# Kernel tuning notes

Measured on AMD Instinct MI355X. Metric: run time of the kernel, lower is better.

## Reference

```python
import jax, jax.numpy as jnp
import numpy as np

NUM_HEADS = 12  # per init_kwargs


def setup_inputs() -> dict:
    key = jax.random.key(0)
    k1, k2, k3 = jax.random.split(key, 3)
    B, H, W, D = 1, 64, 64, 768
    x = jax.random.normal(k1, (B, H, W, D), dtype=jnp.float32)
    # torch nn.Linear weights are [out, in]; small init keeps softmax well-conditioned
    w_qkv = jax.random.normal(k2, (3 * D, D), dtype=jnp.float32) * 0.02
    w_proj = jax.random.normal(k3, (D, D), dtype=jnp.float32) * 0.02
    b_proj = jnp.zeros((D,), dtype=jnp.float32)
    return {"x": x, "w_qkv": w_qkv, "w_proj": w_proj, "b_proj": b_proj}


def reference(x, w_qkv, w_proj, b_proj):
    B, H, W, D = x.shape
    S = H * W
    nh = NUM_HEADS
    hd = D // nh
    scale = hd ** (-0.5)
    # qkv: [B, S, 3, nh, hd] -> q,k,v each [B, nh, S, hd]
    qkv = jnp.einsum('bhwd,ed->bhwe', x, w_qkv).reshape(B, S, 3, nh, hd)
    qkv = jnp.transpose(qkv, (2, 0, 3, 1, 4))
    q, k, v = qkv[0], qkv[1], qkv[2]
    # full O(S^2) attention matrix, as in the original module
    wei = jnp.einsum('bnqd,bnkd->bnqk', q * scale, k)
    wei = jax.nn.softmax(wei, axis=-1)
    # att_drop omitted (eval mode / deterministic baseline)
    out = jnp.einsum('bnqk,bnkd->bnqd', wei, v)  # [B, nh, S, hd]
    # [B, nh, H, W, hd] -> [B, H, W, nh*hd]
    out = jnp.transpose(out.reshape(B, nh, H, W, hd), (0, 2, 3, 1, 4)).reshape(B, H, W, D)
    proj = jnp.einsum('bhwd,ed->bhwe', out, w_proj) + b_proj
    return proj
```

## Files before the change

### kernel.cpp

```cpp
#include <hip/hip_runtime.h>
#include <hip/hip_bf16.h>
#include <math.h>

typedef short s16x8 __attribute__((ext_vector_type(8)));
typedef unsigned u32x2 __attribute__((ext_vector_type(2)));
typedef unsigned u32x4 __attribute__((ext_vector_type(4)));
typedef float f32x4 __attribute__((ext_vector_type(4)));
typedef float f32x16 __attribute__((ext_vector_type(16)));
typedef __hip_bfloat16 bf16;

#define GLD16(g, l)                                                        \
  __builtin_amdgcn_global_load_lds(                                        \
      (const __attribute__((address_space(1))) void*)(g),                  \
      (__attribute__((address_space(3))) void*)(l), 16, 0, 0)

#define MFMA16(a, b, c) __builtin_amdgcn_mfma_f32_16x16x32_bf16((a), (b), (c), 0, 0, 0)
#define MFMA32(a, b, c) __builtin_amdgcn_mfma_f32_32x32x16_bf16((a), (b), (c), 0, 0, 0)

static constexpr int kS = 4096;
static constexpr int kD = 768;
static constexpr int kNH = 12;
static constexpr int kHD = 64;
static constexpr int kNE = 2304;
static constexpr int kNS = 2;

static __device__ __forceinline__ float bf2f(short s) {
  union { unsigned u; float f; } x;
  x.u = ((unsigned)(unsigned short)s) << 16;
  return x.f;
}

static constexpr int kNX8 = kS * kD / 8;
static constexpr int kNWq8 = kNE * kD / 8;
static constexpr int kNWp8 = kD * kD / 8;

__global__ __launch_bounds__(256)
void k_cvt3(const float* __restrict__ x, const float* __restrict__ wq,
            const float* __restrict__ wp, bf16* __restrict__ xb,
            bf16* __restrict__ wqb, bf16* __restrict__ wpb) {
  int i = blockIdx.x * 256 + threadIdx.x;
  const float* src;
  short* dst;
  if (i < kNX8) {
    src = x; dst = (short*)xb;
  } else if (i < kNX8 + kNWq8) {
    i -= kNX8; src = wq; dst = (short*)wqb;
  } else {
    i -= kNX8 + kNWq8; if (i >= kNWp8) return;
    src = wp; dst = (short*)wpb;
  }
  const f32x4 a = *(const f32x4*)(src + i * 8);
  const f32x4 b = *(const f32x4*)(src + i * 8 + 4);
  s16x8 o;
#pragma unroll
  for (int j = 0; j < 4; ++j) {
    o[j] = (short)__bfloat16_as_ushort(__float2bfloat16(a[j]));
    o[j + 4] = (short)__bfloat16_as_ushort(__float2bfloat16(b[j]));
  }
  *(s16x8*)(dst + i * 8) = o;
}

__global__ __launch_bounds__(256, 2)
void k_qkv(const bf16* __restrict__ X, const bf16* __restrict__ W,
           bf16* __restrict__ Qw, bf16* __restrict__ Kw, bf16* __restrict__ Vw) {
  __shared__ __align__(16) short As[2][128 * 32];
  __shared__ __align__(16) short Bs[2][128 * 32];
  const int tid = threadIdx.x;
  const int wv = tid >> 6, ln = tid & 63;
  const int r = ln & 15, kq = ln >> 4;
  const int bm = blockIdx.x * 128;
  const int bn = blockIdx.y * 128;
  const int wr = wv >> 1, wc = wv & 1;
  const short* Xs = (const short*)X;
  const short* Ws = (const short*)W;

  f32x4 acc[4][4] = {};

  const int c0 = wv * 128 + ln, c1 = c0 + 64;
  const int ra0 = c0 >> 2, ka0 = c0 & 3;
  const int ra1 = c1 >> 2, ka1 = c1 & 3;
  const int off0 = wv * 1024, off1 = off0 + 512;
  const short* gA0 = Xs + (bm + ra0) * kD + ka0 * 8;
  const short* gA1 = Xs + (bm + ra1) * kD + ka1 * 8;
  const short* gB0 = Ws + (bn + ra0) * kD + ka0 * 8;
  const short* gB1 = Ws + (bn + ra1) * kD + ka1 * 8;

  GLD16(gA0, &As[0][off0]);
  GLD16(gA1, &As[0][off1]);
  GLD16(gB0, &Bs[0][off0]);
  GLD16(gB1, &Bs[0][off1]);
  __syncthreads();

  const int NT = kD / 32;
  for (int t = 0; t < NT; ++t) {
    const short* aCur = As[t & 1];
    const short* bCur = Bs[t & 1];
    if (t + 1 < NT) {
      const int k1 = (t + 1) * 32;
      short* aN = As[(t + 1) & 1];
      short* bN = Bs[(t + 1) & 1];
      GLD16(gA0 + k1, aN + off0);
      GLD16(gA1 + k1, aN + off1);
      GLD16(gB0 + k1, bN + off0);
      GLD16(gB1 + k1, bN + off1);
    }
    s16x8 a[4], b[4];
#pragma unroll
    for (int i = 0; i < 4; ++i)
      a[i] = *(const s16x8*)(aCur + (wr * 64 + i * 16 + r) * 32 + kq * 8);
#pragma unroll
    for (int j = 0; j < 4; ++j)
      b[j] = *(const s16x8*)(bCur + (wc * 64 + j * 16 + r) * 32 + kq * 8);
#pragma unroll
    for (int i = 0; i < 4; ++i)
#pragma unroll
      for (int j = 0; j < 4; ++j) acc[i][j] = MFMA16(a[i], b[j], acc[i][j]);
    __syncthreads();
  }

  const int which = bn / kD;
  bf16* dst = (which == 0) ? Qw : (which == 1) ? Kw : Vw;
  const float scl = (which == 0) ? 0.125f : 1.0f;
  const int ebase = bn - which * kD + wc * 64;
#pragma unroll
  for (int j = 0; j < 4; ++j) {
    const int e = ebase + j * 16 + r;
    const int h = e >> 6, d = e & 63;
#pragma unroll
    for (int i = 0; i < 4; ++i) {
      const int srow = bm + wr * 64 + i * 16 + kq * 4;
#pragma unroll
      for (int rr = 0; rr < 4; ++rr)
        dst[(h * kS + srow + rr) * kHD + d] = __float2bfloat16(acc[i][j][rr] * scl);
    }
  }
}

__global__ __launch_bounds__(256, 2)
void k_vt(const bf16* __restrict__ Vw, bf16* __restrict__ Vt) {
  __shared__ __align__(16) short L[64 * 72];
  const int h = blockIdx.y, st = blockIdx.x;
  const int t = threadIdx.x;
  const short* src = (const short*)Vw + (h * kS + st * 64) * kHD;
  short* dstb = (short*)Vt + h * kHD * kS;
#pragma unroll
  for (int u = 0; u < 2; ++u) {
    const int c = u * 256 + t;
    const int row = c >> 3, ch = c & 7;
    *(s16x8*)(L + row * 72 + ch * 8) = *(const s16x8*)(src + row * kHD + ch * 8);
  }
  __syncthreads();
#pragma unroll
  for (int u = 0; u < 2; ++u) {
    const int c = u * 256 + t;
    const int d = c >> 3, ch = c & 7;
    s16x8 v;
#pragma unroll
    for (int j = 0; j < 8; ++j) v[j] = L[(ch * 8 + j) * 72 + d];
    *(s16x8*)(dstb + d * kS + st * 64 + ch * 8) = v;
  }
}

__global__ __launch_bounds__(256, 5)
void k_attn(const bf16* __restrict__ Qw, const bf16* __restrict__ Kw,
            const bf16* __restrict__ Vt, bf16* __restrict__ Opart,
            float* __restrict__ Lpart) {
  __shared__ __align__(16) short Ks[2][64 * 64];
  __shared__ __align__(16) short Vs[2][64 * 64];
  const int tid = threadIdx.x;
  const int wv = tid >> 6, ln = tid & 63;
  const int qh = wv >> 1;
  const int kvh = wv & 1;
  const int col = ln & 31;
  const int lh = ln >> 5;

  const int wg = blockIdx.x;
  const int p = (wg & 7) >> 1;
  const int b = ((wg >> 3) << 1) | (wg & 1);
  const int hh = 3 * p + (b >> 7);
  const int rem = b & 127;
  const int qb = rem >> 1;
  const int j = rem & 1;
  const int q0 = qb * 64;
  const int pidx = (hh * 64 + qb) * kNS + j;

  const short* Qh = (const short*)Qw + ((size_t)hh * kS + q0 + qh * 32) * kHD;
  const short* Kh = (const short*)Kw + (size_t)hh * kS * kHD + (size_t)j * 2048 * kHD;
  const short* Vh = (const short*)Vt + (size_t)hh * kHD * kS + j * 2048;

  s16x8 bq[4];
#pragma unroll
  for (int kb = 0; kb < 4; ++kb)
    bq[kb] = *(const s16x8*)(Qh + col * kHD + kb * 16 + lh * 8);

  f32x16 o[2] = {};
  float lp = 0.f;

  int ldso[2];
  const short* gK[2];
  const short* gV[2];
#pragma unroll
  for (int u = 0; u < 2; ++u) {
    const int c = u * 256 + tid;
    const int kr = c >> 3, g = (c & 7) ^ (kr & 7);
    ldso[u] = c * 8;
    gK[u] = Kh + kr * kHD + g * 8;
    gV[u] = Vh + kr * kS + g * 8;
  }

#pragma unroll
  for (int u = 0; u < 2; ++u) {
    GLD16(gK[u], &Ks[0][ldso[u]]);
    GLD16(gV[u], &Vs[0][ldso[u]]);
  }
  __syncthreads();

  const int NT2 = 32;
  for (int kt = 0; kt < NT2; ++kt) {
    const short* ksCur = Ks[kt & 1];
    const short* vsCur = Vs[kt & 1];
    if (kt + 1 < NT2) {
      short* ksN = Ks[(kt + 1) & 1];
      short* vsN = Vs[(kt + 1) & 1];
      const int dk = (kt + 1) * 64 * kHD;
      const int dv = (kt + 1) * 64;
#pragma unroll
      for (int u = 0; u < 2; ++u) {
        GLD16(gK[u] + dk, ksN + ldso[u]);
        GLD16(gV[u] + dv, vsN + ldso[u]);
      }
    }

    f32x16 z = {};
    const int krow = kvh * 32 + col;
    const int ksw = krow & 7;
    __builtin_amdgcn_s_setprio(1);
#pragma unroll
    for (int kb = 0; kb < 4; ++kb) {
      const int ch = ((kb << 1) + lh) ^ ksw;
      s16x8 ak = *(const s16x8*)(ksCur + krow * 64 + ch * 8);
      z = MFMA32(ak, bq[kb], z);
    }
    __builtin_amdgcn_s_setprio(0);

    float pv[16];
#pragma unroll
    for (int g = 0; g < 16; ++g) {
      pv[g] = __expf(z[g]);
      lp += pv[g];
    }
    unsigned own[8];
#pragma unroll
    for (int m = 0; m < 8; ++m) {
      const unsigned f0 = __builtin_bit_cast(unsigned, pv[2 * m]);
      const unsigned f1 = __builtin_bit_cast(unsigned, pv[2 * m + 1]);
      own[m] = __builtin_amdgcn_perm(f1, f0, 0x07060302u);
    }

    __builtin_amdgcn_s_setprio(1);
#pragma unroll
    for (int kvk = 0; kvk < 2; ++kvk) {
      u32x2 sA = __builtin_amdgcn_permlane32_swap(own[4 * kvk + 0], own[4 * kvk + 2], false, false);
      u32x2 sB = __builtin_amdgcn_permlane32_swap(own[4 * kvk + 1], own[4 * kvk + 3], false, false);
      u32x4 apv;
      apv[0] = sA[0];
      apv[1] = sB[0];
      apv[2] = sA[1];
      apv[3] = sB[1];
      const s16x8 ap = __builtin_bit_cast(s16x8, apv);
      const int kvg = kvh * 2 + kvk;
#pragma unroll
      for (int db = 0; db < 2; ++db) {
        const int vrow = db * 32 + col;
        const int ch = ((kvg << 1) + lh) ^ (vrow & 7);
        s16x8 vb = *(const s16x8*)(vsCur + vrow * 64 + ch * 8);
        o[db] = MFMA32(ap, vb, o[db]);
      }
    }
    __builtin_amdgcn_s_setprio(0);
    __syncthreads();
  }

  lp += __shfl_xor(lp, 32);
  float* Of = (float*)Ks;
  float* Lf = (float*)Vs;

  if (kvh == 1) {
#pragma unroll
    for (int db = 0; db < 2; ++db)
#pragma unroll
      for (int g = 0; g < 16; ++g) {
        const int qoff = (g & 3) + 8 * (g >> 2) + 4 * lh;
        Of[(qh * 32 + qoff) * 64 + db * 32 + col] = o[db][g];
      }
    if (lh == 0) Lf[qh * 32 + col] = lp;
  }
  __syncthreads();
  if (kvh == 0) {
    lp += Lf[qh * 32 + col];
    if (lh == 0) Lpart[pidx * 64 + qh * 32 + col] = lp;
    short* Ob = (short*)Opart + (size_t)pidx * 4096;
#pragma unroll
    for (int db = 0; db < 2; ++db)
#pragma unroll
      for (int g = 0; g < 16; ++g) {
        const int qoff = (g & 3) + 8 * (g >> 2) + 4 * lh;
        const float val = o[db][g] + Of[(qh * 32 + qoff) * 64 + db * 32 + col];
        Ob[(qh * 32 + qoff) * 64 + db * 32 + col] =
            (short)__bfloat16_as_ushort(__float2bfloat16(val));
      }
  }
}

__global__ __launch_bounds__(256)
void k_comb(bf16* __restrict__ Opart, const float* __restrict__ Lpart) {
  const int blk = blockIdx.x;
  const int t = threadIdx.x;
  const int q = t >> 2;
  const int dg = t & 3;
  const int p0 = blk * kNS;
  const float inv = 1.0f / (Lpart[p0 * 64 + q] + Lpart[(p0 + 1) * 64 + q]);
  short* s0 = (short*)Opart + (size_t)p0 * 4096 + q * 64 + dg * 16;
  const short* s1 = s0 + 4096;
#pragma unroll
  for (int jj = 0; jj < 2; ++jj) {
    const s16x8 a = *(const s16x8*)(s0 + jj * 8);
    const s16x8 bb = *(const s16x8*)(s1 + jj * 8);
    s16x8 r;
#pragma unroll
    for (int e = 0; e < 8; ++e) {
      const float v = (bf2f(a[e]) + bf2f(bb[e])) * inv;
      r[e] = (short)__bfloat16_as_ushort(__float2bfloat16(v));
    }
    *(s16x8*)(s0 + jj * 8) = r;
  }
}

__global__ __launch_bounds__(256, 3)
void k_proj(const bf16* __restrict__ Opart, const bf16* __restrict__ W,
            const float* __restrict__ Bias, float* __restrict__ Out) {
  __shared__ __align__(16) short As[2][64 * 32];
  __shared__ __align__(16) short Bs[2][64 * 32];
  const int tid = threadIdx.x;
  const int wv = tid >> 6, ln = tid & 63;
  const int r = ln & 15, kq = ln >> 4;
  const int bm = blockIdx.x * 64;
  const int bn = blockIdx.y * 64;
  const int wr = wv >> 1, wc = wv & 1;
  const short* Asrc = (const short*)Opart;
  const short* Wsrc = (const short*)W;

  f32x4 acc[2][2] = {};
  const int c = wv * 64 + ln;
  const int ra = c >> 2, ka = c & 3;
  const int off = wv * 512;
  const int s = bm + ra;
  const int baseQ = (s >> 6) * (kNS * 4096) + (s & 63) * 64;
  const short* gB = Wsrc + (bn + ra) * kD + ka * 8;

  GLD16(Asrc + baseQ + ka * 8, &As[0][off]);
  GLD16(gB, &Bs[0][off]);
  __syncthreads();

  const int NT = kD / 32;
  for (int t = 0; t < NT; ++t) {
    const short* aCur = As[t & 1];
    const short* bCur = Bs[t & 1];
    if (t + 1 < NT) {
      const int tn = t + 1;
      const int aoff = baseQ + (tn >> 1) * (64 * kNS * 4096) +
                       ((tn & 1) * 32 + ka * 8);
      GLD16(Asrc + aoff, &As[tn & 1][off]);
      GLD16(gB + tn * 32, &Bs[tn & 1][off]);
    }
    s16x8 a[2], b[2];
#pragma unroll
    for (int i = 0; i < 2; ++i)
      a[i] = *(const s16x8*)(aCur + (wr * 32 + i * 16 + r) * 32 + kq * 8);
#pragma unroll
    for (int jj = 0; jj < 2; ++jj)
      b[jj] = *(const s16x8*)(bCur + (wc * 32 + jj * 16 + r) * 32 + kq * 8);
#pragma unroll
    for (int i = 0; i < 2; ++i)
#pragma unroll
      for (int jj = 0; jj < 2; ++jj) acc[i][jj] = MFMA16(a[i], b[jj], acc[i][jj]);
    __syncthreads();
  }
#pragma unroll
  for (int jj = 0; jj < 2; ++jj) {
    const int e = bn + wc * 32 + jj * 16 + r;
    const float bv = Bias[e];
#pragma unroll
    for (int i = 0; i < 2; ++i) {
      const int srow = bm + wr * 32 + i * 16 + kq * 4;
#pragma unroll
      for (int rr = 0; rr < 4; ++rr)
        Out[(srow + rr) * kD + e] = acc[i][jj][rr] + bv;
    }
  }
}

extern "C" void kernel_launch(void* const* d_in, const int* in_sizes, int n_in,
                              void* d_out, int out_size, void* d_ws, size_t ws_size,
                              hipStream_t stream) {
  const float* x = (const float*)d_in[0];
  const float* w_qkv = (const float*)d_in[1];
  const float* w_proj = (const float*)d_in[2];
  const float* b_proj = (const float*)d_in[3];
  float* out = (float*)d_out;

  const size_t HS = (size_t)kNH * kS * kHD;
  const int nX = kS * kD;
  const int nWq = kNE * kD;
  const int nWp = kD * kD;

  bf16* Wpb = (bf16*)d_ws;
  bf16* Qw = Wpb + nWp;
  bf16* Kw = Qw + HS;
  bf16* Vt = Kw + HS;
  bf16* Xb = Vt + HS;
  bf16* Wqb = Xb + nX;
  bf16* Vw = Wqb + nWq;
  bf16* Opart = Xb;
  float* Lpart = (float*)((short*)Opart + (size_t)kNS * 768 * 4096);

  const int totalC = kNX8 + kNWq8 + kNWp8;
  k_cvt3<<<(totalC + 255) / 256, 256, 0, stream>>>(x, w_qkv, w_proj, Xb, Wqb, Wpb);

  k_qkv<<<dim3(kS / 128, kNE / 128), 256, 0, stream>>>(Xb, Wqb, Qw, Kw, Vw);
  k_vt<<<dim3(kS / 64, kNH), 256, 0, stream>>>(Vw, Vt);
  k_attn<<<dim3(kNS * (kS / 64) * kNH), 256, 0, stream>>>(Qw, Kw, Vt, Opart, Lpart);
  k_comb<<<dim3((kS / 64) * kNH), 256, 0, stream>>>(Opart, Lpart);
  k_proj<<<dim3(kS / 64, kD / 64), 256, 0, stream>>>(Opart, Wpb, b_proj, out);
}
```

Baseline: 126.8 us.

## Double query rows per attention workgroup to reuse K/V tiles

Each attention workgroup now covers 128 query rows instead of 64, with every wave holding two Q fragments and two output accumulators that share the same K and V fragments loaded from LDS. This halves the grid and the global K/V traffic per query and amortizes LDS reads over twice the MFMA work. The cost is higher register pressure (launch bounds lowered from 5 to 3 waves per SIMD) and fewer workgroups to fill the GPU.

```diff
diff --git a/kernel.cpp b/kernel.cpp
--- a/kernel.cpp
+++ b/kernel.cpp
@@ -161,12 +161,13 @@
   }
 }
 
-__global__ __launch_bounds__(256, 5)
+__global__ __launch_bounds__(256, 3)
 void k_attn(const bf16* __restrict__ Qw, const bf16* __restrict__ Kw,
             const bf16* __restrict__ Vt, bf16* __restrict__ Opart,
             float* __restrict__ Lpart) {
   __shared__ __align__(16) short Ks[2][64 * 64];
   __shared__ __align__(16) short Vs[2][64 * 64];
+  __shared__ float Lsum[128];
   const int tid = threadIdx.x;
   const int wv = tid >> 6, ln = tid & 63;
   const int qh = wv >> 1;
@@ -177,24 +178,26 @@
   const int wg = blockIdx.x;
   const int p = (wg & 7) >> 1;
   const int b = ((wg >> 3) << 1) | (wg & 1);
-  const int hh = 3 * p + (b >> 7);
-  const int rem = b & 127;
+  const int hh = 3 * p + b / 64;
+  const int rem = b % 64;
   const int qb = rem >> 1;
   const int j = rem & 1;
-  const int q0 = qb * 64;
-  const int pidx = (hh * 64 + qb) * kNS + j;
-
-  const short* Qh = (const short*)Qw + ((size_t)hh * kS + q0 + qh * 32) * kHD;
+  const int q0 = qb * 128;
+
+  const short* Qh = (const short*)Qw + ((size_t)hh * kS + q0 + qh * 64) * kHD;
   const short* Kh = (const short*)Kw + (size_t)hh * kS * kHD + (size_t)j * 2048 * kHD;
   const short* Vh = (const short*)Vt + (size_t)hh * kHD * kS + j * 2048;
 
-  s16x8 bq[4];
-#pragma unroll
-  for (int kb = 0; kb < 4; ++kb)
-    bq[kb] = *(const s16x8*)(Qh + col * kHD + kb * 16 + lh * 8);
-
-  f32x16 o[2] = {};
-  float lp = 0.f;
+  s16x8 bq0[4], bq1[4];
+#pragma unroll
+  for (int kb = 0; kb < 4; ++kb) {
+    bq0[kb] = *(const s16x8*)(Qh + (col) * kHD + kb * 16 + lh * 8);
+    bq1[kb] = *(const s16x8*)(Qh + (32 + col) * kHD + kb * 16 + lh * 8);
+  }
+
+  f32x16 o0[2] = {};
+  f32x16 o1[2] = {};
+  float lp0 = 0.f, lp1 = 0.f;
 
   int ldso[2];
   const short* gK[2];
@@ -214,6 +217,9 @@
     GLD16(gV[u], &Vs[0][ldso[u]]);
   }
   __syncthreads();
+
+  const int krow = kvh * 32 + col;
+  const int ksw = krow & 7;
 
   const int NT2 = 32;
   for (int kt = 0; kt < NT2; ++kt) {
@@ -231,59 +237,77 @@
       }
     }
 
-    f32x16 z = {};
-    const int krow = kvh * 32 + col;
-    const int ksw = krow & 7;
+    s16x8 ak[4];
+#pragma unroll
+    for (int kb = 0; kb < 4; ++kb)
+      ak[kb] = *(const s16x8*)(ksCur + krow * 64 + (((kb << 1) + lh) ^ ksw) * 8);
+    f32x16 z0 = {}, z1 = {};
     __builtin_amdgcn_s_setprio(1);
 #pragma unroll
-    for (int kb = 0; kb < 4; ++kb) {
-      const int ch = ((kb << 1) + lh) ^ ksw;
-      s16x8 ak = *(const s16x8*)(ksCur + krow * 64 + ch * 8);
-      z = MFMA32(ak, bq[kb], z);
-    }
+    for (int kb = 0; kb < 4; ++kb) z0 = MFMA32(ak[kb], bq0[kb], z0);
+#pragma unroll
+    for (int kb = 0; kb < 4; ++kb) z1 = MFMA32(ak[kb], bq1[kb], z1);
     __builtin_amdgcn_s_setprio(0);
 
-    float pv[16];
-#pragma unroll
-    for (int g = 0; g < 16; ++g) {
-      pv[g] = __expf(z[g]);
-      lp += pv[g];
-    }
-    unsigned own[8];
-#pragma unroll
-    for (int m = 0; m < 8; ++m) {
-      const unsigned f0 = __builtin_bit_cast(unsigned, pv[2 * m]);
-      const unsigned f1 = __builtin_bit_cast(unsigned, pv[2 * m + 1]);
-      own[m] = __builtin_amdgcn_perm(f1, f0, 0x07060302u);
+    unsigned own0[8], own1[8];
+    {
+      float pv[16];
+#pragma unroll
+      for (int g = 0; g < 16; ++g) {
+        pv[g] = __expf(z0[g]);
+        lp0 += pv[g];
+      }
+#pragma unroll
+      for (int m = 0; m < 8; ++m) {
+        const unsigned f0 = __builtin_bit_cast(unsigned, pv[2 * m]);
+        const unsigned f1 = __builtin_bit_cast(unsigned, pv[2 * m + 1]);
+        own0[m] = __builtin_amdgcn_perm(f1, f0, 0x07060302u);
+      }
+    }
+    {
+      float pv[16];
+#pragma unroll
+      for (int g = 0; g < 16; ++g) {
+        pv[g] = __expf(z1[g]);
+        lp1 += pv[g];
+      }
+#pragma unroll
+      for (int m = 0; m < 8; ++m) {
+        const unsigned f0 = __builtin_bit_cast(unsigned, pv[2 * m]);
+        const unsigned f1 = __builtin_bit_cast(unsigned, pv[2 * m + 1]);
+        own1[m] = __builtin_amdgcn_perm(f1, f0, 0x07060302u);
+      }
     }
 
     __builtin_amdgcn_s_setprio(1);
 #pragma unroll
     for (int kvk = 0; kvk < 2; ++kvk) {
-      u32x2 sA = __builtin_amdgcn_permlane32_swap(own[4 * kvk + 0], own[4 * kvk + 2], false, false);
-      u32x2 sB = __builtin_amdgcn_permlane32_swap(own[4 * kvk + 1], own[4 * kvk + 3], false, false);
-      u32x4 apv;
-      apv[0] = sA[0];
-      apv[1] = sB[0];
-      apv[2] = sA[1];
-      apv[3] = sB[1];
-      const s16x8 ap = __builtin_bit_cast(s16x8, apv);
+      u32x2 sA0 = __builtin_amdgcn_permlane32_swap(own0[4 * kvk + 0], own0[4 * kvk + 2], false, false);
+      u32x2 sB0 = __builtin_amdgcn_permlane32_swap(own0[4 * kvk + 1], own0[4 * kvk + 3], false, false);
+      u32x2 sA1 = __builtin_amdgcn_permlane32_swap(own1[4 * kvk + 0], own1[4 * kvk + 2], false, false);
+      u32x2 sB1 = __builtin_amdgcn_permlane32_swap(own1[4 * kvk + 1], own1[4 * kvk + 3], false, false);
+      u32x4 a0v, a1v;
+      a0v[0] = sA0[0]; a0v[1] = sB0[0]; a0v[2] = sA0[1]; a0v[3] = sB0[1];
+      a1v[0] = sA1[0]; a1v[1] = sB1[0]; a1v[2] = sA1[1]; a1v[3] = sB1[1];
+      const s16x8 ap0 = __builtin_bit_cast(s16x8, a0v);
+      const s16x8 ap1 = __builtin_bit_cast(s16x8, a1v);
       const int kvg = kvh * 2 + kvk;
 #pragma unroll
       for (int db = 0; db < 2; ++db) {
         const int vrow = db * 32 + col;
         const int ch = ((kvg << 1) + lh) ^ (vrow & 7);
         s16x8 vb = *(const s16x8*)(vsCur + vrow * 64 + ch * 8);
-        o[db] = MFMA32(ap, vb, o[db]);
+        o0[db] = MFMA32(ap0, vb, o0[db]);
+        o1[db] = MFMA32(ap1, vb, o1[db]);
       }
     }
     __builtin_amdgcn_s_setprio(0);
     __syncthreads();
   }
 
-  lp += __shfl_xor(lp, 32);
-  float* Of = (float*)Ks;
-  float* Lf = (float*)Vs;
+  lp0 += __shfl_xor(lp0, 32);
+  lp1 += __shfl_xor(lp1, 32);
+  float* myOf = qh ? (float*)Vs : (float*)Ks;
 
   if (kvh == 1) {
 #pragma unroll
@@ -291,23 +315,35 @@
 #pragma unroll
       for (int g = 0; g < 16; ++g) {
         const int qoff = (g & 3) + 8 * (g >> 2) + 4 * lh;
-        Of[(qh * 32 + qoff) * 64 + db * 32 + col] = o[db][g];
-      }
-    if (lh == 0) Lf[qh * 32 + col] = lp;
+        myOf[qoff * 64 + db * 32 + col] = o0[db][g];
+        myOf[(32 + qoff) * 64 + db * 32 + col] = o1[db][g];
+      }
+    if (lh == 0) {
+      Lsum[qh * 64 + col] = lp0;
+      Lsum[qh * 64 + 32 + col] = lp1;
+    }
   }
   __syncthreads();
   if (kvh == 0) {
-    lp += Lf[qh * 32 + col];
-    if (lh == 0) Lpart[pidx * 64 + qh * 32 + col] = lp;
+    lp0 += Lsum[qh * 64 + col];
+    lp1 += Lsum[qh * 64 + 32 + col];
+    const int pidx = (hh * 64 + qb * 2 + qh) * kNS + j;
+    if (lh == 0) {
+      Lpart[pidx * 64 + col] = lp0;
+      Lpart[pidx * 64 + 32 + col] = lp1;
+    }
     short* Ob = (short*)Opart + (size_t)pidx * 4096;
 #pragma unroll
     for (int db = 0; db < 2; ++db)
 #pragma unroll
       for (int g = 0; g < 16; ++g) {
         const int qoff = (g & 3) + 8 * (g >> 2) + 4 * lh;
-        const float val = o[db][g] + Of[(qh * 32 + qoff) * 64 + db * 32 + col];
-        Ob[(qh * 32 + qoff) * 64 + db * 32 + col] =
-            (short)__bfloat16_as_ushort(__float2bfloat16(val));
+        const float v0 = o0[db][g] + myOf[qoff * 64 + db * 32 + col];
+        const float v1 = o1[db][g] + myOf[(32 + qoff) * 64 + db * 32 + col];
+        Ob[qoff * 64 + db * 32 + col] =
+            (short)__bfloat16_as_ushort(__float2bfloat16(v0));
+        Ob[(32 + qoff) * 64 + db * 32 + col] =
+            (short)__bfloat16_as_ushort(__float2bfloat16(v1));
       }
   }
 }
@@ -429,7 +465,7 @@
 
   k_qkv<<<dim3(kS / 128, kNE / 128), 256, 0, stream>>>(Xb, Wqb, Qw, Kw, Vw);
   k_vt<<<dim3(kS / 64, kNH), 256, 0, stream>>>(Vw, Vt);
-  k_attn<<<dim3(kNS * (kS / 64) * kNH), 256, 0, stream>>>(Qw, Kw, Vt, Opart, Lpart);
+  k_attn<<<dim3((kS / 128) * kNH * kNS), 256, 0, stream>>>(Qw, Kw, Vt, Opart, Lpart);
   k_comb<<<dim3((kS / 64) * kNH), 256, 0, stream>>>(Opart, Lpart);
   k_proj<<<dim3(kS / 64, kD / 64), 256, 0, stream>>>(Opart, Wpb, b_proj, out);
 }
```

Result: slower. 138.0 us (+8.8%).

## Remap GEMM blocks per XCD and stage QKV epilogue through LDS for vector stores

Applied to the files above, without the earlier changes.

Both GEMM kernels now use a 1-D grid, and the block index is remapped so that blocks landing on the same XCD (wg & 7) share adjacent M rows. This is meant to improve L2 reuse of the A and B tiles. The QKV epilogue also writes the accumulator tile into the reused LDS buffers and then stores it to global memory as 16-byte vectors, replacing the scattered 2-byte stores. The exchange is an extra LDS round trip plus a barrier, and the remap hard-codes the grid shape, so it depends on the 32x18 and 64x12 tile counts.

```diff
diff --git a/kernel.cpp b/kernel.cpp
--- a/kernel.cpp
+++ b/kernel.cpp
@@ -68,8 +68,15 @@
   const int tid = threadIdx.x;
   const int wv = tid >> 6, ln = tid & 63;
   const int r = ln & 15, kq = ln >> 4;
-  const int bm = blockIdx.x * 128;
-  const int bn = blockIdx.y * 128;
+
+  const int wg = blockIdx.x;
+  const int p = wg & 7;
+  const int idx = wg >> 3;
+  const int bxl = idx / 18;
+  const int byy = idx % 18;
+  const int bm = (p * 4 + bxl) * 128;
+  const int bn = byy * 128;
+
   const int wr = wv >> 1, wc = wv & 1;
   const short* Xs = (const short*)X;
   const short* Ws = (const short*)W;
@@ -121,18 +128,37 @@
   const int which = bn / kD;
   bf16* dst = (which == 0) ? Qw : (which == 1) ? Kw : Vw;
   const float scl = (which == 0) ? 0.125f : 1.0f;
-  const int ebase = bn - which * kD + wc * 64;
-#pragma unroll
-  for (int j = 0; j < 4; ++j) {
-    const int e = ebase + j * 16 + r;
-    const int h = e >> 6, d = e & 63;
-#pragma unroll
-    for (int i = 0; i < 4; ++i) {
-      const int srow = bm + wr * 64 + i * 16 + kq * 4;
-#pragma unroll
-      for (int rr = 0; rr < 4; ++rr)
-        dst[(h * kS + srow + rr) * kHD + d] = __float2bfloat16(acc[i][j][rr] * scl);
-    }
+  const int bnl = bn - which * kD;
+
+  short* AsF = &As[0][0];
+  short* BsF = &Bs[0][0];
+  {
+    short* Cb = wr ? BsF : AsF;
+#pragma unroll
+    for (int j = 0; j < 4; ++j) {
+      const int colc = wc * 64 + j * 16 + r;
+#pragma unroll
+      for (int i = 0; i < 4; ++i) {
+#pragma unroll
+        for (int rr = 0; rr < 4; ++rr) {
+          const int lr = i * 16 + kq * 4 + rr;
+          Cb[lr * 128 + colc] =
+              (short)__bfloat16_as_ushort(__float2bfloat16(acc[i][j][rr] * scl));
+        }
+      }
+    }
+  }
+  __syncthreads();
+#pragma unroll
+  for (int u = 0; u < 8; ++u) {
+    const int g2 = u * 256 + tid;
+    const int row = g2 >> 4, pos = g2 & 15;
+    const int el = pos * 8;
+    const int h = (bnl >> 6) + (el >> 6);
+    const int d = el & 63;
+    const short* src = ((row < 64) ? AsF : BsF) + (row & 63) * 128 + el;
+    const s16x8 v = *(const s16x8*)src;
+    *(s16x8*)((short*)dst + ((size_t)h * kS + bm + row) * kHD + d) = v;
   }
 }
 
@@ -344,8 +370,15 @@
   const int tid = threadIdx.x;
   const int wv = tid >> 6, ln = tid & 63;
   const int r = ln & 15, kq = ln >> 4;
-  const int bm = blockIdx.x * 64;
-  const int bn = blockIdx.y * 64;
+
+  const int wg = blockIdx.x;
+  const int p = wg & 7;
+  const int idx = wg >> 3;
+  const int bxl = idx / 12;
+  const int byy = idx % 12;
+  const int bm = (p * 8 + bxl) * 64;
+  const int bn = byy * 64;
+
   const int wr = wv >> 1, wc = wv & 1;
   const short* Asrc = (const short*)Opart;
   const short* Wsrc = (const short*)W;
@@ -427,9 +460,9 @@
   const int totalC = kNX8 + kNWq8 + kNWp8;
   k_cvt3<<<(totalC + 255) / 256, 256, 0, stream>>>(x, w_qkv, w_proj, Xb, Wqb, Wpb);
 
-  k_qkv<<<dim3(kS / 128, kNE / 128), 256, 0, stream>>>(Xb, Wqb, Qw, Kw, Vw);
+  k_qkv<<<dim3((kS / 128) * (kNE / 128)), 256, 0, stream>>>(Xb, Wqb, Qw, Kw, Vw);
   k_vt<<<dim3(kS / 64, kNH), 256, 0, stream>>>(Vw, Vt);
   k_attn<<<dim3(kNS * (kS / 64) * kNH), 256, 0, stream>>>(Qw, Kw, Vt, Opart, Lpart);
   k_comb<<<dim3((kS / 64) * kNH), 256, 0, stream>>>(Opart, Lpart);
-  k_proj<<<dim3(kS / 64, kD / 64), 256, 0, stream>>>(Opart, Wpb, b_proj, out);
-}
+  k_proj<<<dim3((kS / 64) * (kD / 64)), 256, 0, stream>>>(Opart, Wpb, b_proj, out);
+}
```

Result: slower. 129.7 us (+2.3%).
